# Kernel optimization log

Hardware: AMD Instinct MI355X
Metric: run time of the kernel (lower is better)

## Reference

```python
import jax, jax.numpy as jnp
import numpy as np

DAMPING_PARAM = 0.7
N_NODES = 100000
N_EDGES = 6400000


def setup_inputs() -> dict:
    key = jax.random.key(0)
    k1, k2, k3, k4, k5, k6, k7 = jax.random.split(key, 7)
    species = jax.random.randint(k1, (N_NODES,), 0, 10, dtype=jnp.int32)
    edge_src = jax.random.randint(k2, (N_EDGES,), 0, N_NODES, dtype=jnp.int32)
    edge_dst = jax.random.randint(k3, (N_EDGES,), 0, N_NODES, dtype=jnp.int32)
    # distances strictly positive (avoid division by ~0 in 1/r^3)
    distances = jax.random.uniform(k4, (N_EDGES,), dtype=jnp.float32) * 4.0 + 0.5
    vec = jax.random.normal(k5, (N_EDGES, 3), dtype=jnp.float32)
    charges = jax.random.normal(k6, (N_NODES,), dtype=jnp.float32)
    # polarisability strictly positive (raised to fractional power)
    polarisability = jax.random.uniform(k7, (N_NODES,), dtype=jnp.float32) * 2.0 + 0.5
    return {
        "species": species,
        "edge_src": edge_src,
        "edge_dst": edge_dst,
        "distances": distances,
        "vec": vec,
        "charges": charges,
        "polarisability": polarisability,
    }


def reference(species, edge_src, edge_dst, distances, vec, charges, polarisability):
    # Testing path ('training_flag' not in inputs): all Au.BOHR conversions cancel.
    n_nodes = species.shape[0]
    rij = distances  # [E]
    q_ij = charges[edge_dst]  # [E] gather
    alpha_ij = polarisability[edge_src] * polarisability[edge_dst]  # [E]
    uij = rij / alpha_ij ** (1.0 / 6.0)  # [E]
    damping = 1.0 - jnp.exp(-DAMPING_PARAM * uij ** 1.5)  # [E]
    # eij = -q_j * vec_ij / r^3 * damping  -> [E, 3]
    coeff = -q_ij * damping / rij ** 3  # [E]
    eij = coeff[:, None] * vec  # [E, 3]
    electric_field = jax.ops.segment_sum(eij, edge_src, num_segments=n_nodes)  # [N, 3]
    return electric_field.reshape(-1)  # [N*3]
```

## Files before the change

### kernel.cpp

```cpp
#include <hip/hip_runtime.h>
#include <hip/hip_fp16.h>
#include <cmath>

#define DAMPING 0.7f
#define NBUCKETS 64
#define NPB 1563
#define KSLOT 3
#define CHUNK 4096
#define CAP 112
#define NCOPIES 32
#define BLOCK 256
#define BLOCK2 512
#define EPT 8


union h2u {
    __half2 h;
    unsigned u;
};

__device__ __forceinline__ uint2 pack_rec(float ex, float ey, float ez,
                                          int li) {
    h2u lo;
    lo.h = __floats2half2_rn(ex, ey);
    unsigned hi = (unsigned)__half_as_ushort(__float2half_rn(ez)) |
                  ((unsigned)li << 16);
    return make_uint2(lo.u, hi);
}

__device__ __forceinline__ void unpack(uint2 r, float& x, float& y, float& z) {
    h2u lo;
    lo.u = r.x;
    x = __low2float(lo.h);
    y = __high2float(lo.h);
    z = __half2float(__ushort_as_half((unsigned short)(r.y & 0xFFFFu)));
}


__global__ __launch_bounds__(256) void table_kernel(
    const float* __restrict__ polar, const float* __restrict__ charges,
    float2* __restrict__ cd, int n) {
    int i = blockIdx.x * blockDim.x + threadIdx.x;
    if (i < n) cd[i] = make_float2(charges[i], powf(polar[i], 1.0f / 6.0f));
}

__global__ __launch_bounds__(256) void pass1_kernel(
    const int* __restrict__ esrc, const int* __restrict__ edst,
    const float* __restrict__ dist, const float* __restrict__ vec,
    const float2* __restrict__ cd, uint2* __restrict__ regions,
    unsigned* __restrict__ counts, int n_edges) {
    __shared__ unsigned gcur[NBUCKETS];
    const int c = blockIdx.x;
    const long base0 = (long)c * CHUNK;
    if (threadIdx.x < NBUCKETS) gcur[threadIdx.x] = 0u;
    __syncthreads();
    uint2* __restrict__ myreg = regions + (long)c * NBUCKETS * CAP;

    for (int t0 = 0; t0 < CHUNK; t0 += BLOCK * EPT) {
        const long e0 = base0 + t0 + (long)threadIdx.x * EPT;
        if (e0 + EPT <= n_edges) {
            int4 sA = *reinterpret_cast<const int4*>(esrc + e0);
            int4 sB = *reinterpret_cast<const int4*>(esrc + e0 + 4);
            int4 dA = *reinterpret_cast<const int4*>(edst + e0);
            int4 dB = *reinterpret_cast<const int4*>(edst + e0 + 4);
            float4 rA = *reinterpret_cast<const float4*>(dist + e0);
            float4 rB = *reinterpret_cast<const float4*>(dist + e0 + 4);
            float4 v0 = *reinterpret_cast<const float4*>(vec + 3 * e0);
            float4 v1 = *reinterpret_cast<const float4*>(vec + 3 * e0 + 4);
            float4 v2 = *reinterpret_cast<const float4*>(vec + 3 * e0 + 8);
            float4 v3 = *reinterpret_cast<const float4*>(vec + 3 * e0 + 12);
            float4 v4 = *reinterpret_cast<const float4*>(vec + 3 * e0 + 16);
            float4 v5 = *reinterpret_cast<const float4*>(vec + 3 * e0 + 20);
            int s[EPT] = {sA.x, sA.y, sA.z, sA.w, sB.x, sB.y, sB.z, sB.w};
            int d[EPT] = {dA.x, dA.y, dA.z, dA.w, dB.x, dB.y, dB.z, dB.w};
            float r[EPT] = {rA.x, rA.y, rA.z, rA.w, rB.x, rB.y, rB.z, rB.w};
            float v[3 * EPT] = {v0.x, v0.y, v0.z, v0.w, v1.x, v1.y, v1.z,
                                v1.w, v2.x, v2.y, v2.z, v2.w, v3.x, v3.y,
                                v3.z, v3.w, v4.x, v4.y, v4.z, v4.w, v5.x,
                                v5.y, v5.z, v5.w};
            float2 cs[EPT], cdd[EPT];
#pragma unroll
            for (int k = 0; k < EPT; ++k) cs[k] = cd[s[k]];
#pragma unroll
            for (int k = 0; k < EPT; ++k) cdd[k] = cd[d[k]];
            uint2 rec[EPT];
            int b[EPT];
#pragma unroll
            for (int k = 0; k < EPT; ++k) {
                float a6 = cs[k].y * cdd[k].y;
                float rr = r[k];
                float u = rr / a6;
                float damp = 1.0f - __expf(-DAMPING * u * sqrtf(u));
                float coeff = -cdd[k].x * damp / (rr * rr * rr);
                b[k] = s[k] / NPB;
                int li = s[k] - b[k] * NPB;
                rec[k] = pack_rec(coeff * v[3 * k + 0], coeff * v[3 * k + 1],
                                  coeff * v[3 * k + 2], li);
            }
            unsigned slot[EPT];
#pragma unroll
            for (int k = 0; k < EPT; ++k) slot[k] = atomicAdd(&gcur[b[k]], 1u);
#pragma unroll
            for (int k = 0; k < EPT; ++k)
                if (slot[k] < (unsigned)CAP)
                    myreg[b[k] * CAP + slot[k]] = rec[k];
        } else {
            for (long e = e0; e < e0 + EPT && e < n_edges; ++e) {
                int s = esrc[e];
                int d = edst[e];
                float2 cs = cd[s];
                float2 cdd = cd[d];
                float a6 = cs.y * cdd.y;
                float rr = dist[e];
                float u = rr / a6;
                float damp = 1.0f - __expf(-DAMPING * u * sqrtf(u));
                float coeff = -cdd.x * damp / (rr * rr * rr);
                int b = s / NPB;
                int li = s - b * NPB;
                uint2 rec =
                    pack_rec(coeff * vec[3 * e + 0], coeff * vec[3 * e + 1],
                             coeff * vec[3 * e + 2], li);
                unsigned slot = atomicAdd(&gcur[b], 1u);
                if (slot < (unsigned)CAP) myreg[b * CAP + slot] = rec;
            }
        }
    }
    __syncthreads();
    if (threadIdx.x < NBUCKETS)
        counts[c * NBUCKETS + threadIdx.x] =
            min(gcur[threadIdx.x], (unsigned)CAP);
}

__global__ __launch_bounds__(512) void pass2_kernel(
    const uint2* __restrict__ regions, const unsigned* __restrict__ counts,
    float* __restrict__ copies, int nchunks, int n_nodes) {
    __shared__ unsigned cnt[NPB];
    __shared__ uint2 sorted[KSLOT * NPB];
    __shared__ float accOv[NPB * 3];
    __shared__ unsigned scounts[64];
    const int b = blockIdx.x >> 5;
    const int k = blockIdx.x & 31;
    const int nstrips = (nchunks - k + NCOPIES - 1) / NCOPIES;
    for (int j = threadIdx.x; j < NPB; j += BLOCK2) cnt[j] = 0u;
    for (int j = threadIdx.x; j < NPB * 3; j += BLOCK2) accOv[j] = 0.f;
    if (threadIdx.x < nstrips)
        scounts[threadIdx.x] =
            counts[(long)(k + threadIdx.x * NCOPIES) * NBUCKETS + b];
    __syncthreads();
    const int wave = threadIdx.x >> 6;
    const int lane = threadIdx.x & 63;
    const unsigned i0 = (unsigned)lane;
    const unsigned i1 = (unsigned)min(lane + 64, CAP - 1);
    for (int j0 = wave; j0 < nstrips; j0 += 32) {
        uint2 r[8];
        unsigned n[4];
#pragma unroll
        for (int t = 0; t < 4; ++t) {
            int j = j0 + 8 * t;
            int jc = (j < nstrips) ? j : j0;
            n[t] = (j < nstrips) ? scounts[jc] : 0u;
            const uint2* rg =
                regions + ((long)(k + (long)jc * NCOPIES) * NBUCKETS + b) * CAP;
            r[2 * t] = rg[i0];
            r[2 * t + 1] = rg[i1];
        }
#pragma unroll
        for (int t = 0; t < 4; ++t) {
#pragma unroll
            for (int hh = 0; hh < 2; ++hh) {
                unsigned idx = (unsigned)lane + 64u * hh;
                if (idx < n[t]) {
                    uint2 rr = r[2 * t + hh];
                    int li = (int)(rr.y >> 16);
                    unsigned slot = atomicAdd(&cnt[li], 1u);
                    if (slot < (unsigned)KSLOT) {
                        sorted[slot * NPB + li] = rr;
                    } else {
                        float x, y, z;
                        unpack(rr, x, y, z);
                        atomicAdd(&accOv[li * 3 + 0], x);
                        atomicAdd(&accOv[li * 3 + 1], y);
                        atomicAdd(&accOv[li * 3 + 2], z);
                    }
                }
            }
        }
    }
    __syncthreads();
    float* __restrict__ plane = copies + (long)k * (3L * n_nodes);
#pragma unroll
    for (int jj = 0; jj < 4; ++jj) {
        int li = (int)threadIdx.x + jj * BLOCK2;
        if (li < NPB) {
            float ax = accOv[li * 3 + 0];
            float ay = accOv[li * 3 + 1];
            float az = accOv[li * 3 + 2];
            unsigned c = min(cnt[li], (unsigned)KSLOT);
#pragma unroll
            for (unsigned s = 0; s < (unsigned)KSLOT; ++s) {
                if (s < c) {
                    float x, y, z;
                    unpack(sorted[s * NPB + li], x, y, z);
                    ax += x;
                    ay += y;
                    az += z;
                }
            }
            int g = b * NPB + li;
            if (g < n_nodes) {
                long base = 3L * g;
                plane[base + 0] = ax;
                plane[base + 1] = ay;
                plane[base + 2] = az;
            }
        }
    }
}

__global__ __launch_bounds__(256) void reduce_kernel(
    const float4* __restrict__ copies, float4* __restrict__ out, int total4) {
    int t = blockIdx.x * blockDim.x + threadIdx.x;
    if (t < total4) {
        float4 s = make_float4(0.f, 0.f, 0.f, 0.f);
#pragma unroll
        for (int k = 0; k < NCOPIES; ++k) {
            float4 v = copies[(long)k * total4 + t];
            s.x += v.x; s.y += v.y; s.z += v.z; s.w += v.w;
        }
        out[t] = s;
    }
}


__global__ __launch_bounds__(256) void edge_scatter_direct_kernel(
    const int* __restrict__ esrc, const int* __restrict__ edst,
    const float* __restrict__ dist, const float* __restrict__ vec,
    const float* __restrict__ charges, const float* __restrict__ polar,
    float* __restrict__ out, int n_edges) {
    int e = blockIdx.x * blockDim.x + threadIdx.x;
    if (e >= n_edges) return;
    float a6 = powf(polar[esrc[e]] * polar[edst[e]], 1.0f / 6.0f);
    float rr = dist[e];
    float u = rr / a6;
    float damp = 1.0f - expf(-DAMPING * u * sqrtf(u));
    float coeff = -charges[edst[e]] * damp / (rr * rr * rr);
    int base = 3 * esrc[e];
    unsafeAtomicAdd(out + base + 0, coeff * vec[3 * (long)e + 0]);
    unsafeAtomicAdd(out + base + 1, coeff * vec[3 * (long)e + 1]);
    unsafeAtomicAdd(out + base + 2, coeff * vec[3 * (long)e + 2]);
}

extern "C" void kernel_launch(void* const* d_in, const int* in_sizes, int n_in,
                              void* d_out, int out_size, void* d_ws, size_t ws_size,
                              hipStream_t stream) {
    const int* edge_src = (const int*)d_in[1];
    const int* edge_dst = (const int*)d_in[2];
    const float* distances = (const float*)d_in[3];
    const float* vec = (const float*)d_in[4];
    const float* charges = (const float*)d_in[5];
    const float* polar = (const float*)d_in[6];
    float* out = (float*)d_out;

    const int n_edges = in_sizes[1];
    const int n_nodes = in_sizes[0];
    const int nchunks = (n_edges + CHUNK - 1) / CHUNK;

    auto align = [](size_t x) { return (x + 4095) & ~(size_t)4095; };
    size_t off_cd = 0;
    size_t cd_bytes = align((size_t)n_nodes * sizeof(float2));
    size_t off_counts = off_cd + cd_bytes;
    size_t counts_bytes = align((size_t)nchunks * NBUCKETS * sizeof(unsigned));
    size_t off_regions = off_counts + counts_bytes;
    size_t regions_bytes =
        align((size_t)nchunks * NBUCKETS * CAP * sizeof(uint2));
    size_t off_copies = off_regions + regions_bytes;
    size_t copies_bytes =
        (size_t)NCOPIES * 3 * (size_t)n_nodes * sizeof(float);
    size_t need = off_copies + copies_bytes;

    bool main_path = (n_nodes <= NBUCKETS * NPB) &&
                     ((long)nchunks * CHUNK >= n_edges) && (ws_size >= need) &&
                     (nchunks <= NCOPIES * 64) && (CHUNK == 2 * BLOCK * EPT) &&
                     ((3 * n_nodes) % 4 == 0);

    if (main_path) {
        float2* cd = (float2*)((char*)d_ws + off_cd);
        unsigned* counts = (unsigned*)((char*)d_ws + off_counts);
        uint2* regions = (uint2*)((char*)d_ws + off_regions);
        float* copies = (float*)((char*)d_ws + off_copies);

        table_kernel<<<(n_nodes + BLOCK - 1) / BLOCK, BLOCK, 0, stream>>>(
            polar, charges, cd, n_nodes);
        pass1_kernel<<<nchunks, BLOCK, 0, stream>>>(
            edge_src, edge_dst, distances, vec, cd, regions, counts, n_edges);
        pass2_kernel<<<NBUCKETS * NCOPIES, BLOCK2, 0, stream>>>(
            regions, counts, copies, nchunks, n_nodes);
        reduce_kernel<<<((3 * n_nodes / 4) + BLOCK - 1) / BLOCK, BLOCK, 0,
                        stream>>>(
            (const float4*)copies, (float4*)out, 3 * n_nodes / 4);
    } else {
        hipMemsetAsync(d_out, 0, (size_t)out_size * sizeof(float), stream);
        edge_scatter_direct_kernel<<<(n_edges + BLOCK - 1) / BLOCK, BLOCK, 0,
                                     stream>>>(
            edge_src, edge_dst, distances, vec, charges, polar, out, n_edges);
    }
}
```

Baseline: 291.6 us.

## Stage bucketed records in shared memory and flush coalesced per bucket

Pass1 no longer scatters each packed edge record straight to global memory. Each record first goes into a per-bucket LDS staging buffer (64 buckets × 56 slots), and after each 2048-edge sub-tile the waves flush the staged records to the chunk's global regions with contiguous, lane-strided stores. Records that overflow a bucket's staging depth still go directly to global memory. A sched_barrier is also added after the gathers to constrain instruction scheduling. The aim is to replace scattered 8-byte stores with coalesced writes, at the cost of two extra block barriers per sub-tile and about 28KB of LDS, which may reduce occupancy.

```diff
diff --git a/kernel.cpp b/kernel.cpp
--- a/kernel.cpp
+++ b/kernel.cpp
@@ -8,6 +8,7 @@
 #define KSLOT 3
 #define CHUNK 4096
 #define CAP 112
+#define DEPTH 56
 #define NCOPIES 32
 #define BLOCK 256
 #define BLOCK2 512
@@ -49,10 +50,15 @@
     const float* __restrict__ dist, const float* __restrict__ vec,
     const float2* __restrict__ cd, uint2* __restrict__ regions,
     unsigned* __restrict__ counts, int n_edges) {
+    __shared__ uint2 stage[NBUCKETS][DEPTH];
+    __shared__ unsigned scnt[NBUCKETS];
     __shared__ unsigned gcur[NBUCKETS];
     const int c = blockIdx.x;
     const long base0 = (long)c * CHUNK;
-    if (threadIdx.x < NBUCKETS) gcur[threadIdx.x] = 0u;
+    if (threadIdx.x < NBUCKETS) {
+        scnt[threadIdx.x] = 0u;
+        gcur[threadIdx.x] = 0u;
+    }
     __syncthreads();
     uint2* __restrict__ myreg = regions + (long)c * NBUCKETS * CAP;
 
@@ -83,6 +89,7 @@
             for (int k = 0; k < EPT; ++k) cs[k] = cd[s[k]];
 #pragma unroll
             for (int k = 0; k < EPT; ++k) cdd[k] = cd[d[k]];
+            __builtin_amdgcn_sched_barrier(0);
             uint2 rec[EPT];
             int b[EPT];
 #pragma unroll
@@ -97,13 +104,16 @@
                 rec[k] = pack_rec(coeff * v[3 * k + 0], coeff * v[3 * k + 1],
                                   coeff * v[3 * k + 2], li);
             }
-            unsigned slot[EPT];
-#pragma unroll
-            for (int k = 0; k < EPT; ++k) slot[k] = atomicAdd(&gcur[b[k]], 1u);
-#pragma unroll
-            for (int k = 0; k < EPT; ++k)
-                if (slot[k] < (unsigned)CAP)
-                    myreg[b[k] * CAP + slot[k]] = rec[k];
+#pragma unroll
+            for (int k = 0; k < EPT; ++k) {
+                unsigned slot = atomicAdd(&scnt[b[k]], 1u);
+                if (slot < (unsigned)DEPTH) {
+                    stage[b[k]][slot] = rec[k];
+                } else {
+                    unsigned gd = gcur[b[k]] + slot;
+                    if (gd < (unsigned)CAP) myreg[b[k] * CAP + gd] = rec[k];
+                }
+            }
         } else {
             for (long e = e0; e < e0 + EPT && e < n_edges; ++e) {
                 int s = esrc[e];
@@ -120,15 +130,40 @@
                 uint2 rec =
                     pack_rec(coeff * vec[3 * e + 0], coeff * vec[3 * e + 1],
                              coeff * vec[3 * e + 2], li);
-                unsigned slot = atomicAdd(&gcur[b], 1u);
-                if (slot < (unsigned)CAP) myreg[b * CAP + slot] = rec;
-            }
-        }
-    }
-    __syncthreads();
+                unsigned slot = atomicAdd(&scnt[b], 1u);
+                if (slot < (unsigned)DEPTH) {
+                    stage[b][slot] = rec;
+                } else {
+                    unsigned gd = gcur[b] + slot;
+                    if (gd < (unsigned)CAP) myreg[b * CAP + gd] = rec;
+                }
+            }
+        }
+        __syncthreads();
+        {
+            const int wave = threadIdx.x >> 6;
+            const int lane = threadIdx.x & 63;
+#pragma unroll
+            for (int rr = 0; rr < 16; ++rr) {
+                int b = wave * 16 + rr;
+                unsigned full = scnt[b];
+                unsigned n = min(full, (unsigned)DEPTH);
+                unsigned g = gcur[b];
+                uint2* dst = myreg + b * CAP;
+                for (unsigned i = lane; i < n; i += 64) {
+                    unsigned o = g + i;
+                    if (o < (unsigned)CAP) dst[o] = stage[b][i];
+                }
+                if (lane == 0) {
+                    gcur[b] = min(g + full, (unsigned)CAP);
+                    scnt[b] = 0u;
+                }
+            }
+        }
+        __syncthreads();
+    }
     if (threadIdx.x < NBUCKETS)
-        counts[c * NBUCKETS + threadIdx.x] =
-            min(gcur[threadIdx.x], (unsigned)CAP);
+        counts[c * NBUCKETS + threadIdx.x] = gcur[threadIdx.x];
 }
 
 __global__ __launch_bounds__(512) void pass2_kernel(
```

Result: faster. 268.7 us (median of 2 runs) (-7.9%).
